# Performance work log

Hardware: AMD Instinct MI355X
Metric: run time of the kernel (lower is better)

## Reference

```python
import jax, jax.numpy as jnp
import numpy as np

H, W, A = 1024, 1024, 64

def setup_inputs() -> dict:
    key = jax.random.key(0)
    k0, k1, k2, k3 = jax.random.split(key, 4)
    field = jax.random.normal(k0, (H, W), dtype=jnp.float32)
    signal = jax.random.normal(k1, (H, W), dtype=jnp.float32)
    attractor_pos = jax.random.randint(k2, (A, 2), 0, H)  # (i, j) centers
    attractor_strength = jax.random.uniform(k3, (A,), jnp.float32, 0.5, 3.0)
    return {
        "field": field,
        "signal": signal,
        "attractor_pos": attractor_pos,
        "attractor_strength": attractor_strength,
        "influence_strength": jnp.float32(0.5),  # 'challenge' signal -> challenge_influence init
        "global_ratio": jnp.float32(0.3),
        "local_ratio": jnp.float32(0.7),
    }


def _influence_map(shape, attractor_pos, attractor_strength, global_ratio, local_ratio):
    h, w = shape
    ii = jnp.arange(h)[None, :, None]  # [1,H,1]
    jj = jnp.arange(w)[None, None, :]  # [1,1,W]
    di = ii - attractor_pos[:, 0][:, None, None]  # [A,H,W]
    dj = jj - attractor_pos[:, 1][:, None, None]  # [A,H,W]
    s = attractor_strength[:, None, None]  # [A,1,1]
    radius = jnp.floor(5.0 * s)  # int(5*strength), square window cutoff
    mask = (jnp.abs(di) <= radius) & (jnp.abs(dj) <= radius)
    d2 = (di * di + dj * dj).astype(jnp.float32)
    falloff = jnp.exp(-0.5 * d2 / (4.0 * s * s))  # (dist/(2*strength))^2
    contrib = jnp.sum(jnp.where(mask, falloff * local_ratio * s, 0.0), axis=0)  # [H,W]
    im = jax.nn.sigmoid(global_ratio + contrib)
    return jnp.clip(im, 0.0, 1.0)


def reference(field, signal, attractor_pos, attractor_strength, influence_strength, global_ratio, local_ratio):
    im = _influence_map(field.shape, attractor_pos, attractor_strength, global_ratio, local_ratio)
    a = im * influence_strength
    upd = field * (1.0 - a) + signal * a
    n = jnp.linalg.norm(upd)
    upd = jnp.where(n > 0, upd * (jnp.linalg.norm(field) / n), upd)
    return upd
```

## Files before the change

kernel.cpp:

```cpp
#include <hip/hip_runtime.h>

#define HH 1024
#define WW 1024
#define NA 64
#define NBLK1 512
#define NBLK2 512


__global__ __launch_bounds__(256) void frp_fused(
    const float4* __restrict__ field,
    const float4* __restrict__ signal,
    const int*   __restrict__ apos,
    const float* __restrict__ astr,
    const float* __restrict__ p_is,
    const float* __restrict__ p_gr,
    const float* __restrict__ p_lr,
    float4* __restrict__ out,
    float2* __restrict__ part)
{
    __shared__ int   s_pj[2][NA];
    __shared__ int   s_rad[2][NA];
    __shared__ int   s_di2[2][NA];
    __shared__ float s_coef[2][NA];
    __shared__ float s_inv[2][NA];
    __shared__ int   s_nact[2];
    __shared__ float s_part[2][4];

    const float lr = *p_lr;
    const float gr = *p_gr;
    const float is = *p_is;

    const int t    = threadIdx.x;
    const int row0 = blockIdx.x * 2;

    if (t < NA) {
        float s  = astr[t];
        int   pi = apos[2 * t + 0];
        int   pj = apos[2 * t + 1];
        int   r  = (int)floorf(5.0f * s);
        float cf = lr * s;
        float iv = -0.125f / (s * s);
#pragma unroll
        for (int rr = 0; rr < 2; ++rr) {
            int di = (row0 + rr) - pi;
            bool active = (di >= -r && di <= r);
            unsigned long long mask = __ballot(active);
            int pos = __popcll(mask & ((1ull << t) - 1ull));
            if (active) {
                s_pj[rr][pos]   = pj;
                s_rad[rr][pos]  = r;
                s_di2[rr][pos]  = di * di;
                s_coef[rr][pos] = cf;
                s_inv[rr][pos]  = iv;
            }
            if (t == 0) s_nact[rr] = __popcll(mask);
        }
    }
    __syncthreads();

    const int half = t >> 7;
    const int tt   = t & 127;
    const int row  = row0 + half;
    const int col0 = tt << 3;
    const int n    = s_nact[half];

    float c[8] = {0,0,0,0,0,0,0,0};
    for (int k = 0; k < n; ++k) {
        int   pj  = s_pj[half][k];
        int   r   = s_rad[half][k];
        int   di2 = s_di2[half][k];
        float cf  = s_coef[half][k];
        float iv  = s_inv[half][k];
#pragma unroll
        for (int q = 0; q < 8; ++q) {
            int dj = col0 + q - pj;
            if (dj >= -r && dj <= r)
                c[q] += cf * __expf(iv * (float)(di2 + dj * dj));
        }
    }

    const int idx = row * (WW / 4) + (tt << 1);
    float4 f0  = field[idx];
    float4 f1  = field[idx + 1];
    float4 g0  = signal[idx];
    float4 g1  = signal[idx + 1];

    float a[8];
#pragma unroll
    for (int q = 0; q < 8; ++q)
        a[q] = is / (1.0f + __expf(-(gr + c[q])));

    float4 u0, u1;
    u0.x = f0.x + (g0.x - f0.x) * a[0];
    u0.y = f0.y + (g0.y - f0.y) * a[1];
    u0.z = f0.z + (g0.z - f0.z) * a[2];
    u0.w = f0.w + (g0.w - f0.w) * a[3];
    u1.x = f1.x + (g1.x - f1.x) * a[4];
    u1.y = f1.y + (g1.y - f1.y) * a[5];
    u1.z = f1.z + (g1.z - f1.z) * a[6];
    u1.w = f1.w + (g1.w - f1.w) * a[7];
    out[idx]     = u0;
    out[idx + 1] = u1;

    float sf = f0.x*f0.x + f0.y*f0.y + f0.z*f0.z + f0.w*f0.w
             + f1.x*f1.x + f1.y*f1.y + f1.z*f1.z + f1.w*f1.w;
    float su = u0.x*u0.x + u0.y*u0.y + u0.z*u0.z + u0.w*u0.w
             + u1.x*u1.x + u1.y*u1.y + u1.z*u1.z + u1.w*u1.w;
#pragma unroll
    for (int off = 32; off > 0; off >>= 1) {
        sf += __shfl_down(sf, off, 64);
        su += __shfl_down(su, off, 64);
    }
    const int wave = t >> 6;
    if ((t & 63) == 0) {
        s_part[0][wave] = sf;
        s_part[1][wave] = su;
    }
    __syncthreads();
    if (t == 0) {
        part[blockIdx.x] = make_float2(
            s_part[0][0] + s_part[0][1] + s_part[0][2] + s_part[0][3],
            s_part[1][0] + s_part[1][1] + s_part[1][2] + s_part[1][3]);
    }
}

__global__ __launch_bounds__(256) void frp_scale(
    float4* __restrict__ out,
    const float2* __restrict__ part)
{
    __shared__ double sp[2][4];
    __shared__ float  s_scale;
    const int t = threadIdx.x;

    const float4* p4 = (const float4*)part;
    float4 v = p4[t];

    const int idx = blockIdx.x * 512 + (t << 1);
    float4 o0 = out[idx];
    float4 o1 = out[idx + 1];

    double df = (double)v.x + (double)v.z;
    double du = (double)v.y + (double)v.w;
#pragma unroll
    for (int off = 32; off > 0; off >>= 1) {
        df += __shfl_down(df, off, 64);
        du += __shfl_down(du, off, 64);
    }
    const int wave = t >> 6;
    if ((t & 63) == 0) { sp[0][wave] = df; sp[1][wave] = du; }
    __syncthreads();
    if (t == 0) {
        double tf = sp[0][0] + sp[0][1] + sp[0][2] + sp[0][3];
        double tu = sp[1][0] + sp[1][1] + sp[1][2] + sp[1][3];
        s_scale = (tu > 0.0) ? (float)sqrt(tf / tu) : 1.0f;
    }
    __syncthreads();

    const float s = s_scale;
    o0.x *= s; o0.y *= s; o0.z *= s; o0.w *= s;
    o1.x *= s; o1.y *= s; o1.z *= s; o1.w *= s;
    out[idx]     = o0;
    out[idx + 1] = o1;
}

extern "C" void kernel_launch(void* const* d_in, const int* in_sizes, int n_in,
                              void* d_out, int out_size, void* d_ws, size_t ws_size,
                              hipStream_t stream) {
    const float4* field  = (const float4*)d_in[0];
    const float4* signal = (const float4*)d_in[1];
    const int*    apos   = (const int*)d_in[2];
    const float*  astr   = (const float*)d_in[3];
    const float*  p_is   = (const float*)d_in[4];
    const float*  p_gr   = (const float*)d_in[5];
    const float*  p_lr   = (const float*)d_in[6];

    float2* part = (float2*)d_ws;

    frp_fused<<<NBLK1, 256, 0, stream>>>(
        field, signal, apos, astr, p_is, p_gr, p_lr,
        (float4*)d_out, part);

    frp_scale<<<NBLK2, 256, 0, stream>>>(
        (float4*)d_out, part);
}
```

Measured before the change: 13.37 us.

## Fuse norm rescale into single kernel with hierarchical atomic grid barrier

Replaces the two-kernel sequence (compute + partial norms, then rescale) with one persistent kernel of 128 blocks, each handling 8 rows and keeping its results in registers. A two-level atomic counter picks the last block, which reduces the partial sums and publishes the scale through per-group flags. The other blocks spin on those flags and then write the scaled output, so the second launch and the re-read of the output are gone. In exchange the work is split across fewer blocks, a memset is added per call, and correctness depends on all 128 blocks being resident at once, since the waiting blocks spin.

```diff
diff --git a/kernel.cpp b/kernel.cpp
--- a/kernel.cpp
+++ b/kernel.cpp
@@ -3,11 +3,13 @@
 #define HH 1024
 #define WW 1024
 #define NA 64
-#define NBLK1 512
-#define NBLK2 512
-
-
-__global__ __launch_bounds__(256) void frp_fused(
+#define NBLK 128
+#define NGRP 8
+#define GSIZE (NBLK / NGRP)
+
+#define WS_CTRL_BYTES (128 * 17)
+
+__global__ __launch_bounds__(256) void frp_one(
     const float4* __restrict__ field,
     const float4* __restrict__ signal,
     const int*   __restrict__ apos,
@@ -16,96 +18,113 @@
     const float* __restrict__ p_gr,
     const float* __restrict__ p_lr,
     float4* __restrict__ out,
+    unsigned* __restrict__ wsi,
     float2* __restrict__ part)
 {
-    __shared__ int   s_pj[2][NA];
-    __shared__ int   s_rad[2][NA];
-    __shared__ int   s_di2[2][NA];
-    __shared__ float s_coef[2][NA];
-    __shared__ float s_inv[2][NA];
-    __shared__ int   s_nact[2];
-    __shared__ float s_part[2][4];
+    __shared__ int    s_pj[2][NA];
+    __shared__ int    s_rad[2][NA];
+    __shared__ int    s_di2[2][NA];
+    __shared__ float  s_coef[2][NA];
+    __shared__ float  s_inv[2][NA];
+    __shared__ int    s_nact[2];
+    __shared__ float  s_part[2][4];
+    __shared__ double s_red[2][4];
+    __shared__ int    s_last;
+    __shared__ unsigned s_bits;
 
     const float lr = *p_lr;
     const float gr = *p_gr;
     const float is = *p_is;
 
     const int t    = threadIdx.x;
-    const int row0 = blockIdx.x * 2;
-
-    if (t < NA) {
-        float s  = astr[t];
-        int   pi = apos[2 * t + 0];
-        int   pj = apos[2 * t + 1];
-        int   r  = (int)floorf(5.0f * s);
-        float cf = lr * s;
-        float iv = -0.125f / (s * s);
-#pragma unroll
-        for (int rr = 0; rr < 2; ++rr) {
-            int di = (row0 + rr) - pi;
-            bool active = (di >= -r && di <= r);
-            unsigned long long mask = __ballot(active);
-            int pos = __popcll(mask & ((1ull << t) - 1ull));
-            if (active) {
-                s_pj[rr][pos]   = pj;
-                s_rad[rr][pos]  = r;
-                s_di2[rr][pos]  = di * di;
-                s_coef[rr][pos] = cf;
-                s_inv[rr][pos]  = iv;
-            }
-            if (t == 0) s_nact[rr] = __popcll(mask);
-        }
-    }
-    __syncthreads();
+    const int b    = blockIdx.x;
+    const int row0 = b * 8;
 
     const int half = t >> 7;
     const int tt   = t & 127;
-    const int row  = row0 + half;
     const int col0 = tt << 3;
-    const int n    = s_nact[half];
-
-    float c[8] = {0,0,0,0,0,0,0,0};
-    for (int k = 0; k < n; ++k) {
-        int   pj  = s_pj[half][k];
-        int   r   = s_rad[half][k];
-        int   di2 = s_di2[half][k];
-        float cf  = s_coef[half][k];
-        float iv  = s_inv[half][k];
-#pragma unroll
-        for (int q = 0; q < 8; ++q) {
-            int dj = col0 + q - pj;
-            if (dj >= -r && dj <= r)
-                c[q] += cf * __expf(iv * (float)(di2 + dj * dj));
-        }
-    }
-
-    const int idx = row * (WW / 4) + (tt << 1);
-    float4 f0  = field[idx];
-    float4 f1  = field[idx + 1];
-    float4 g0  = signal[idx];
-    float4 g1  = signal[idx + 1];
-
-    float a[8];
-#pragma unroll
-    for (int q = 0; q < 8; ++q)
-        a[q] = is / (1.0f + __expf(-(gr + c[q])));
-
-    float4 u0, u1;
-    u0.x = f0.x + (g0.x - f0.x) * a[0];
-    u0.y = f0.y + (g0.y - f0.y) * a[1];
-    u0.z = f0.z + (g0.z - f0.z) * a[2];
-    u0.w = f0.w + (g0.w - f0.w) * a[3];
-    u1.x = f1.x + (g1.x - f1.x) * a[4];
-    u1.y = f1.y + (g1.y - f1.y) * a[5];
-    u1.z = f1.z + (g1.z - f1.z) * a[6];
-    u1.w = f1.w + (g1.w - f1.w) * a[7];
-    out[idx]     = u0;
-    out[idx + 1] = u1;
-
-    float sf = f0.x*f0.x + f0.y*f0.y + f0.z*f0.z + f0.w*f0.w
-             + f1.x*f1.x + f1.y*f1.y + f1.z*f1.z + f1.w*f1.w;
-    float su = u0.x*u0.x + u0.y*u0.y + u0.z*u0.z + u0.w*u0.w
-             + u1.x*u1.x + u1.y*u1.y + u1.z*u1.z + u1.w*u1.w;
+
+    float4 ua0, ub0, ua1, ub1, ua2, ub2, ua3, ub3;
+    float sf = 0.f, su = 0.f;
+
+#pragma unroll
+    for (int p = 0; p < 4; ++p) {
+        if (p > 0) __syncthreads();
+        if (t < NA) {
+            float s  = astr[t];
+            int   pi = apos[2 * t + 0];
+            int   pj = apos[2 * t + 1];
+            int   r  = (int)floorf(5.0f * s);
+            float cf = lr * s;
+            float iv = -0.125f / (s * s);
+#pragma unroll
+            for (int rr = 0; rr < 2; ++rr) {
+                int di = (row0 + 2 * p + rr) - pi;
+                bool active = (di >= -r && di <= r);
+                unsigned long long mask = __ballot(active);
+                int pos = __popcll(mask & ((1ull << t) - 1ull));
+                if (active) {
+                    s_pj[rr][pos]   = pj;
+                    s_rad[rr][pos]  = r;
+                    s_di2[rr][pos]  = di * di;
+                    s_coef[rr][pos] = cf;
+                    s_inv[rr][pos]  = iv;
+                }
+                if (t == 0) s_nact[rr] = __popcll(mask);
+            }
+        }
+        __syncthreads();
+
+        const int row = row0 + 2 * p + half;
+        const int n   = s_nact[half];
+
+        float c[8] = {0,0,0,0,0,0,0,0};
+        for (int k = 0; k < n; ++k) {
+            int   pj  = s_pj[half][k];
+            int   r   = s_rad[half][k];
+            int   di2 = s_di2[half][k];
+            float cf  = s_coef[half][k];
+            float iv  = s_inv[half][k];
+#pragma unroll
+            for (int q = 0; q < 8; ++q) {
+                int dj = col0 + q - pj;
+                if (dj >= -r && dj <= r)
+                    c[q] += cf * __expf(iv * (float)(di2 + dj * dj));
+            }
+        }
+
+        const int idx = row * (WW / 4) + (tt << 1);
+        float4 f0 = field[idx];
+        float4 f1 = field[idx + 1];
+        float4 g0 = signal[idx];
+        float4 g1 = signal[idx + 1];
+
+        float a[8];
+#pragma unroll
+        for (int q = 0; q < 8; ++q)
+            a[q] = is / (1.0f + __expf(-(gr + c[q])));
+
+        float4 u0, u1;
+        u0.x = f0.x + (g0.x - f0.x) * a[0];
+        u0.y = f0.y + (g0.y - f0.y) * a[1];
+        u0.z = f0.z + (g0.z - f0.z) * a[2];
+        u0.w = f0.w + (g0.w - f0.w) * a[3];
+        u1.x = f1.x + (g1.x - f1.x) * a[4];
+        u1.y = f1.y + (g1.y - f1.y) * a[5];
+        u1.z = f1.z + (g1.z - f1.z) * a[6];
+        u1.w = f1.w + (g1.w - f1.w) * a[7];
+
+        if (p == 0) { ua0 = u0; ub0 = u1; }
+        if (p == 1) { ua1 = u0; ub1 = u1; }
+        if (p == 2) { ua2 = u0; ub2 = u1; }
+        if (p == 3) { ua3 = u0; ub3 = u1; }
+
+        sf += f0.x*f0.x + f0.y*f0.y + f0.z*f0.z + f0.w*f0.w
+            + f1.x*f1.x + f1.y*f1.y + f1.z*f1.z + f1.w*f1.w;
+        su += u0.x*u0.x + u0.y*u0.y + u0.z*u0.z + u0.w*u0.w
+            + u1.x*u1.x + u1.y*u1.y + u1.z*u1.z + u1.w*u1.w;
+    }
+
 #pragma unroll
     for (int off = 32; off > 0; off >>= 1) {
         sf += __shfl_down(sf, off, 64);
@@ -117,50 +136,91 @@
         s_part[1][wave] = su;
     }
     __syncthreads();
+
     if (t == 0) {
-        part[blockIdx.x] = make_float2(
+        part[b] = make_float2(
             s_part[0][0] + s_part[0][1] + s_part[0][2] + s_part[0][3],
             s_part[1][0] + s_part[1][1] + s_part[1][2] + s_part[1][3]);
-    }
-}
-
-__global__ __launch_bounds__(256) void frp_scale(
-    float4* __restrict__ out,
-    const float2* __restrict__ part)
-{
-    __shared__ double sp[2][4];
-    __shared__ float  s_scale;
-    const int t = threadIdx.x;
-
-    const float4* p4 = (const float4*)part;
-    float4 v = p4[t];
-
-    const int idx = blockIdx.x * 512 + (t << 1);
-    float4 o0 = out[idx];
-    float4 o1 = out[idx + 1];
-
-    double df = (double)v.x + (double)v.z;
-    double du = (double)v.y + (double)v.w;
-#pragma unroll
-    for (int off = 32; off > 0; off >>= 1) {
-        df += __shfl_down(df, off, 64);
-        du += __shfl_down(du, off, 64);
-    }
-    const int wave = t >> 6;
-    if ((t & 63) == 0) { sp[0][wave] = df; sp[1][wave] = du; }
+        __threadfence();
+        const int g = b >> 4;
+        unsigned old = atomicAdd(&wsi[32 * (1 + g)], 1u);
+        int last = 0;
+        if (old == GSIZE - 1) {
+            __threadfence();
+            unsigned o2 = atomicAdd(&wsi[0], 1u);
+            if (o2 == NGRP - 1) last = 1;
+        }
+        s_last = last;
+    }
     __syncthreads();
-    if (t == 0) {
-        double tf = sp[0][0] + sp[0][1] + sp[0][2] + sp[0][3];
-        double tu = sp[1][0] + sp[1][1] + sp[1][2] + sp[1][3];
-        s_scale = (tu > 0.0) ? (float)sqrt(tf / tu) : 1.0f;
-    }
-    __syncthreads();
-
-    const float s = s_scale;
-    o0.x *= s; o0.y *= s; o0.z *= s; o0.w *= s;
-    o1.x *= s; o1.y *= s; o1.z *= s; o1.w *= s;
-    out[idx]     = o0;
-    out[idx + 1] = o1;
+
+    if (s_last) {
+        __threadfence();
+        double df = 0.0, du = 0.0;
+        if (t < NBLK) {
+            unsigned long long pv = __hip_atomic_load(
+                (const unsigned long long*)(part + t),
+                __ATOMIC_RELAXED, __HIP_MEMORY_SCOPE_AGENT);
+            float2 p2;
+            __builtin_memcpy(&p2, &pv, 8);
+            df = (double)p2.x;
+            du = (double)p2.y;
+        }
+#pragma unroll
+        for (int off = 32; off > 0; off >>= 1) {
+            df += __shfl_down(df, off, 64);
+            du += __shfl_down(du, off, 64);
+        }
+        if ((t & 63) == 0) { s_red[0][wave] = df; s_red[1][wave] = du; }
+        __syncthreads();
+        if (t == 0) {
+            double tf = s_red[0][0] + s_red[0][1] + s_red[0][2] + s_red[0][3];
+            double tu = s_red[1][0] + s_red[1][1] + s_red[1][2] + s_red[1][3];
+            float scale = (tu > 0.0) ? (float)sqrt(tf / tu) : 1.0f;
+            s_bits = __float_as_uint(scale);
+        }
+        __syncthreads();
+        if (t < NGRP)
+            __hip_atomic_store(&wsi[32 * (9 + t)], s_bits,
+                               __ATOMIC_RELAXED, __HIP_MEMORY_SCOPE_AGENT);
+    } else {
+        if (t == 0) {
+            const unsigned* fl = &wsi[32 * (9 + (b & 7))];
+            unsigned v = __hip_atomic_load(fl, __ATOMIC_RELAXED,
+                                           __HIP_MEMORY_SCOPE_AGENT);
+            if (v == 0u) {
+                __builtin_amdgcn_s_sleep(4);
+                v = __hip_atomic_load(fl, __ATOMIC_RELAXED, __HIP_MEMORY_SCOPE_AGENT);
+            }
+            if (v == 0u) {
+                __builtin_amdgcn_s_sleep(8);
+                v = __hip_atomic_load(fl, __ATOMIC_RELAXED, __HIP_MEMORY_SCOPE_AGENT);
+            }
+            if (v == 0u) {
+                __builtin_amdgcn_s_sleep(16);
+                v = __hip_atomic_load(fl, __ATOMIC_RELAXED, __HIP_MEMORY_SCOPE_AGENT);
+            }
+            while (v == 0u) {
+                __builtin_amdgcn_s_sleep(32);
+                v = __hip_atomic_load(fl, __ATOMIC_RELAXED, __HIP_MEMORY_SCOPE_AGENT);
+            }
+            s_bits = v;
+        }
+        __syncthreads();
+    }
+
+    const float sc = __uint_as_float(s_bits);
+#pragma unroll
+    for (int p = 0; p < 4; ++p) {
+        const int row = row0 + 2 * p + half;
+        const int idx = row * (WW / 4) + (tt << 1);
+        float4 u0 = (p == 0) ? ua0 : (p == 1) ? ua1 : (p == 2) ? ua2 : ua3;
+        float4 u1 = (p == 0) ? ub0 : (p == 1) ? ub1 : (p == 2) ? ub2 : ub3;
+        u0.x *= sc; u0.y *= sc; u0.z *= sc; u0.w *= sc;
+        u1.x *= sc; u1.y *= sc; u1.z *= sc; u1.w *= sc;
+        out[idx]     = u0;
+        out[idx + 1] = u1;
+    }
 }
 
 extern "C" void kernel_launch(void* const* d_in, const int* in_sizes, int n_in,
@@ -174,12 +234,12 @@
     const float*  p_gr   = (const float*)d_in[5];
     const float*  p_lr   = (const float*)d_in[6];
 
-    float2* part = (float2*)d_ws;
-
-    frp_fused<<<NBLK1, 256, 0, stream>>>(
+    unsigned* wsi  = (unsigned*)d_ws;
+    float2*   part = (float2*)((char*)d_ws + WS_CTRL_BYTES);
+
+    hipMemsetAsync(d_ws, 0, WS_CTRL_BYTES, stream);
+
+    frp_one<<<NBLK, 256, 0, stream>>>(
         field, signal, apos, astr, p_is, p_gr, p_lr,
-        (float4*)d_out, part);
-
-    frp_scale<<<NBLK2, 256, 0, stream>>>(
-        (float4*)d_out, part);
+        (float4*)d_out, wsi, part);
 }
```

Result: slower. 26.49 us (+98.2%).
